# Performance work log

Measured on AMD Instinct MI355X. Metric: run time of the kernel, lower is better.

The kernel has to match this reference:

```python
import jax, jax.numpy as jnp
import numpy as np

N = 100000
F_IN = 128
DIM = 2
E = 3200000


def setup_inputs() -> dict:
    key = jax.random.key(0)
    k1, k2, k3, k4, k5, k6, k7 = jax.random.split(key, 7)
    x = jax.random.normal(k1, (N, F_IN), dtype=jnp.float32)
    edge_index = jax.random.randint(k2, (2, E), 0, N, dtype=jnp.int64)
    edge_attr = jax.random.uniform(k3, (E,), dtype=jnp.float32)
    # GCNConv params: lin weight [F_IN, DIM] (glorot), bias zeros
    conv_w = jax.random.normal(k4, (F_IN, DIM), dtype=jnp.float32) * (1.0 / np.sqrt(F_IN))
    conv_b = jnp.zeros((DIM,), dtype=jnp.float32)
    # TopKPooling score weight [DIM]
    pool_w = jax.random.normal(k5, (DIM,), dtype=jnp.float32)
    # fc: Linear(N*DIM, 1), init normal(0, 0.01), bias 0 (per init_weights)
    fc_w = jax.random.normal(k6, (N * DIM, 1), dtype=jnp.float32) * 0.01
    fc_b = jnp.zeros((1,), dtype=jnp.float32)
    return {"x": x, "edge_index": edge_index, "edge_attr": edge_attr,
            "conv_w": conv_w, "conv_b": conv_b, "pool_w": pool_w,
            "fc_w": fc_w, "fc_b": fc_b}


def reference(x, edge_index, edge_attr, conv_w, conv_b, pool_w, fc_w, fc_b):
    n = x.shape[0]
    row, col = edge_index[0], edge_index[1]
    # --- GCNConv: add self-loops (weight 1), symmetric normalization ---
    loop = jnp.arange(n, dtype=edge_index.dtype)
    row_f = jnp.concatenate([row, loop])
    col_f = jnp.concatenate([col, loop])
    w_f = jnp.concatenate([edge_attr, jnp.ones((n,), dtype=x.dtype)])
    deg = jax.ops.segment_sum(w_f, col_f, num_segments=n)  # [N]
    dinv = jnp.where(deg > 0, jax.lax.rsqrt(deg), 0.0)
    norm = dinv[row_f] * w_f * dinv[col_f]  # [E+N]
    h = x @ conv_w  # [N, DIM] transform-then-propagate
    msg = norm[:, None] * h[row_f]  # [E+N, DIM]
    out = jax.ops.segment_sum(msg, col_f, num_segments=n) + conv_b  # [N, DIM]
    # --- ReLU ---
    out = jax.nn.relu(out)
    # --- TopKPooling with k = N (single graph): score, sort desc, gate ---
    score = jnp.tanh((out @ pool_w) / jnp.linalg.norm(pool_w))  # [N]
    perm = jnp.argsort(-score)
    pooled = out[perm] * score[perm][:, None]  # [N, DIM]
    # --- flatten + fc + sigmoid ---
    flat = pooled.reshape(-1)  # [N*DIM]
    y = jax.nn.sigmoid(flat @ fc_w + fc_b)  # [1]
    return y
```

## Files before the change

### kernel.cpp

```cpp
#include <hip/hip_runtime.h>
#include <math.h>

#define FIN 128
#define W 512
#define MAXG 256
#define HB 256
#define HT 1024
#define BP 100

__device__ __forceinline__ long long edge_at(const void* p, long long i, unsigned mode) {
  return mode ? ((const long long*)p)[i] : (long long)((const int*)p)[i];
}

__device__ __forceinline__ void atomic_fadd(float* p, float v) {
  __hip_atomic_fetch_add(p, v, __ATOMIC_RELAXED, __HIP_MEMORY_SCOPE_AGENT);
}

__global__ void k_detect(const unsigned* ei, unsigned* mode, float* acc) {
  if (threadIdx.x == 0 && blockIdx.x == 0) {
    unsigned orv = 0;
    for (int i = 1; i < 1024; i += 2) orv |= ei[i];
    *mode = (orv == 0) ? 1u : 0u;
    *acc = 0.0f;
  }
}

__global__ void k_h(const float* __restrict__ x, const float* __restrict__ cw,
                    float* __restrict__ h, int n) {
  int gt = blockIdx.x * blockDim.x + threadIdx.x;
  int node = gt >> 5;
  int sub = gt & 31;
  if (node >= n) return;
  float4 xv = ((const float4*)x)[node * 32 + sub];
  float s0 = xv.x * cw[sub * 8 + 0] + xv.y * cw[sub * 8 + 2] +
             xv.z * cw[sub * 8 + 4] + xv.w * cw[sub * 8 + 6];
  float s1 = xv.x * cw[sub * 8 + 1] + xv.y * cw[sub * 8 + 3] +
             xv.z * cw[sub * 8 + 5] + xv.w * cw[sub * 8 + 7];
  for (int off = 16; off > 0; off >>= 1) {
    s0 += __shfl_down(s0, off, 32);
    s1 += __shfl_down(s1, off, 32);
  }
  if (sub == 0) { h[node * 2] = s0; h[node * 2 + 1] = s1; }
}

__global__ void k_hist(const void* ei, long long E, int G,
                       unsigned* table, const unsigned* __restrict__ mode) {
  __shared__ unsigned hist[MAXG];
  unsigned m = *mode;
  int t = threadIdx.x;
  if (t < MAXG) hist[t] = 0;
  __syncthreads();
  long long perB = (E + HB - 1) / HB;
  long long base = (long long)blockIdx.x * perB;
  long long lim = base + perB; if (lim > E) lim = E;
  for (long long e = base + t; e < lim; e += HT) {
    int c = (int)edge_at(ei, E + e, m);
    atomicAdd(&hist[c >> 9], 1u);
  }
  __syncthreads();
  if (t < G) table[(size_t)t * HB + blockIdx.x] = hist[t];
}

__global__ void k_bsum(const unsigned* __restrict__ table, unsigned* btot) {
  int b = blockIdx.x, t = threadIdx.x;
  unsigned v = table[(size_t)b * HB + t];
  for (int off = 32; off > 0; off >>= 1) v += __shfl_down(v, off);
  __shared__ unsigned wsum[4];
  if ((t & 63) == 0) wsum[t >> 6] = v;
  __syncthreads();
  if (t == 0) btot[b] = wsum[0] + wsum[1] + wsum[2] + wsum[3];
}

__global__ void k_bscan(const unsigned* __restrict__ btot, unsigned* boff,
                        int G, int chunk, unsigned total) {
  __shared__ unsigned part[256];
  int t = threadIdx.x;
  int c0 = t * chunk, c1 = c0 + chunk; if (c1 > G) c1 = G;
  unsigned s = 0;
  for (int i = c0; i < c1; ++i) s += btot[i];
  part[t] = s;
  __syncthreads();
  unsigned pre = 0;
  for (int i = 0; i < t; ++i) pre += part[i];
  unsigned run = pre;
  for (int i = c0; i < c1; ++i) { boff[i] = run; run += btot[i]; }
  if (t == 255) boff[G] = total;
}

__global__ void k_bapply(unsigned* table, const unsigned* __restrict__ boff) {
  __shared__ unsigned s[256];
  int b = blockIdx.x, t = threadIdx.x;
  unsigned v = table[(size_t)b * HB + t];
  s[t] = v;
  __syncthreads();
  for (int off = 1; off < 256; off <<= 1) {
    unsigned tmp = (t >= off) ? s[t - off] : 0u;
    __syncthreads();
    s[t] += tmp;
    __syncthreads();
  }
  table[(size_t)b * HB + t] = s[t] - v + boff[b];
}

__global__ void k_scatter(const void* ei, const float* __restrict__ attr,
                          long long E, int G, const unsigned* __restrict__ table,
                          uint2* __restrict__ packed, const unsigned* __restrict__ mode) {
  __shared__ unsigned cur[MAXG];
  unsigned m = *mode;
  int t = threadIdx.x;
  if (t < G) cur[t] = table[(size_t)t * HB + blockIdx.x];
  __syncthreads();
  long long perB = (E + HB - 1) / HB;
  long long base = (long long)blockIdx.x * perB;
  long long lim = base + perB; if (lim > E) lim = E;
  for (long long e = base + t; e < lim; e += HT) {
    int r = (int)edge_at(ei, e, m);
    int c = (int)edge_at(ei, E + e, m);
    float a = attr[e];
    unsigned pos = atomicAdd(&cur[c >> 9], 1u);
    packed[pos] = make_uint2(((unsigned)r << 9) | ((unsigned)c & 511u), __float_as_uint(a));
  }
}

__global__ void k_gdeg(const uint2* __restrict__ packed, const unsigned* __restrict__ boff,
                       float* __restrict__ deg, int n) {
  __shared__ float sdeg[W];
  int g = blockIdx.x, t = threadIdx.x;
  sdeg[t] = 1.0f;
  __syncthreads();
  unsigned s0 = boff[g], s1 = boff[g + 1];
  for (unsigned i = s0 + t; i < s1; i += W) {
    uint2 p = packed[i];
    atomicAdd(&sdeg[p.x & (W - 1u)], __uint_as_float(p.y));
  }
  __syncthreads();
  int c = g * W + t;
  if (c < n) deg[c] = sdeg[t];
}

__global__ void k_dinv(const float* __restrict__ deg, const float* __restrict__ h,
                       float* __restrict__ dinv, float* __restrict__ g, int n) {
  int i = blockIdx.x * blockDim.x + threadIdx.x;
  if (i >= n) return;
  float di = rsqrtf(deg[i]);
  dinv[i] = di;
  g[2 * i]     = di * h[2 * i];
  g[2 * i + 1] = di * h[2 * i + 1];
}

__global__ void k_gmsg(const uint2* __restrict__ packed, const unsigned* __restrict__ boff,
                       const float* __restrict__ gv, const float* __restrict__ dinv,
                       const float* __restrict__ h, const float* __restrict__ cb,
                       const float* __restrict__ pw, float* __restrict__ out,
                       float* __restrict__ score, unsigned* __restrict__ keys,
                       unsigned* __restrict__ pay, int n) {
  __shared__ float sacc[2 * W];
  int g = blockIdx.x, t = threadIdx.x;
  sacc[t] = 0.f; sacc[t + W] = 0.f;
  __syncthreads();
  unsigned s0 = boff[g], s1 = boff[g + 1];
  const float2* g2 = (const float2*)gv;
  for (unsigned i = s0 + t; i < s1; i += W) {
    uint2 p = packed[i];
    unsigned r = p.x >> 9;
    unsigned cl = p.x & (W - 1u);
    float a = __uint_as_float(p.y);
    float2 gr = g2[r];
    atomicAdd(&sacc[2 * cl],     a * gr.x);
    atomicAdd(&sacc[2 * cl + 1], a * gr.y);
  }
  __syncthreads();
  int c = g * W + t;
  if (c < n) {
    float dc = dinv[c];
    float o0 = fmaxf(dc * sacc[2 * t]     + dc * dc * h[2 * c]     + cb[0], 0.f);
    float o1 = fmaxf(dc * sacc[2 * t + 1] + dc * dc * h[2 * c + 1] + cb[1], 0.f);
    out[2 * c] = o0; out[2 * c + 1] = o1;
    float pw0 = pw[0], pw1 = pw[1];
    float s = tanhf((o0 * pw0 + o1 * pw1) / sqrtf(pw0 * pw0 + pw1 * pw1));
    score[c] = s;
    unsigned u = __float_as_uint(s);
    unsigned asc = u ^ ((u >> 31) ? 0xFFFFFFFFu : 0x80000000u);
    keys[c] = ~asc;
    pay[c] = (unsigned)c;
  }
}

__global__ void k_radix_hist(const unsigned* __restrict__ keys, int n, int shift,
                             unsigned* table) {
  __shared__ unsigned hist[256];
  int t = threadIdx.x;
  hist[t] = 0;
  __syncthreads();
  int base = blockIdx.x * 1024;
  for (int j = 0; j < 4; ++j) {
    int g = base + j * 256 + t;
    if (g < n) {
      unsigned d = (keys[g] >> shift) & 255u;
      atomicAdd(&hist[d], 1u);
    }
  }
  __syncthreads();
  table[t * BP + blockIdx.x] = hist[t];
}

__global__ void k_radix_scan(unsigned* table, int B) {
  int t = threadIdx.x;
  unsigned* row = table + t * BP;
  uint4* r4 = (uint4*)row;
  int nv = B >> 2;
  unsigned s = 0;
#pragma unroll 8
  for (int i = 0; i < nv; ++i) { uint4 v = r4[i]; s += v.x + v.y + v.z + v.w; }
  for (int i = nv * 4; i < B; ++i) s += row[i];
  int lane = t & 63, w = t >> 6;
  unsigned inc = s;
  for (int off = 1; off < 64; off <<= 1) {
    unsigned nval = __shfl_up(inc, off);
    if (lane >= off) inc += nval;
  }
  __shared__ unsigned wtot[4];
  if (lane == 63) wtot[w] = inc;
  __syncthreads();
  unsigned wpre = 0;
  for (int i = 0; i < w; ++i) wpre += wtot[i];
  unsigned run = wpre + inc - s;
#pragma unroll 8
  for (int i = 0; i < nv; ++i) {
    uint4 v = r4[i]; uint4 o;
    o.x = run; run += v.x; o.y = run; run += v.y;
    o.z = run; run += v.z; o.w = run; run += v.w;
    r4[i] = o;
  }
  for (int i = nv * 4; i < B; ++i) { unsigned v = row[i]; row[i] = run; run += v; }
}

__global__ void k_radix_scatter(const unsigned* __restrict__ keysIn,
                                const unsigned* __restrict__ payIn, int n, int shift,
                                const unsigned* __restrict__ table,
                                unsigned* keysOut, unsigned* payOut) {
  __shared__ unsigned runCnt[256];
  __shared__ unsigned waveCnt[4 * 256];
  int t = threadIdx.x;
  int lane = t & 63, w = t >> 6;
  runCnt[t] = 0;
  int base = blockIdx.x * 1024;
  for (int j = 0; j < 4; ++j) {
    for (int q = t; q < 1024; q += 256) waveCnt[q] = 0;
    __syncthreads();
    int g = base + j * 256 + t;
    bool active = g < n;
    unsigned key = 0, pay = 0, d = 0;
    if (active) { key = keysIn[g]; pay = payIn[g]; d = (key >> shift) & 255u; }
    unsigned long long am = __ballot(active);
    unsigned long long mm = ~0ull;
#pragma unroll
    for (int b = 0; b < 8; ++b) {
      unsigned long long bb = __ballot((d >> b) & 1u);
      mm &= ((d >> b) & 1u) ? bb : ~bb;
    }
    mm &= am;
    int rankw = __popcll(mm & ((1ull << lane) - 1ull));
    if (active && rankw == 0) waveCnt[w * 256 + d] = (unsigned)__popcll(mm);
    __syncthreads();
    if (active) {
      unsigned off = runCnt[d] + (unsigned)rankw;
      for (int ww = 0; ww < w; ++ww) off += waveCnt[ww * 256 + d];
      unsigned gpos = table[d * BP + blockIdx.x] + off;
      keysOut[gpos] = key;
      payOut[gpos] = pay;
    }
    __syncthreads();
    runCnt[t] += waveCnt[t] + waveCnt[256 + t] + waveCnt[512 + t] + waveCnt[768 + t];
    __syncthreads();
  }
}

__global__ void k_final(const unsigned* __restrict__ perm, const float* __restrict__ out,
                        const float* __restrict__ score, const float* __restrict__ fcw,
                        float* acc, int n) {
  int stride = gridDim.x * blockDim.x;
  float s = 0.f;
  for (int j = blockIdx.x * blockDim.x + threadIdx.x; j < n; j += stride) {
    unsigned p = perm[j];
    float sc = score[p];
    s += sc * (out[2 * p] * fcw[2 * j] + out[2 * p + 1] * fcw[2 * j + 1]);
  }
  for (int off = 32; off > 0; off >>= 1) s += __shfl_down(s, off);
  if ((threadIdx.x & 63) == 0) atomic_fadd(acc, s);
}

__global__ void k_sigmoid(const float* acc, const float* __restrict__ fcb, float* y) {
  if (threadIdx.x == 0 && blockIdx.x == 0) {
    float z = *acc + fcb[0];
    y[0] = 1.f / (1.f + expf(-z));
  }
}

extern "C" void kernel_launch(void* const* d_in, const int* in_sizes, int n_in,
                              void* d_out, int out_size, void* d_ws, size_t ws_size,
                              hipStream_t stream) {
  const float* x     = (const float*)d_in[0];
  const void*  ei    = d_in[1];
  const float* attr  = (const float*)d_in[2];
  const float* convw = (const float*)d_in[3];
  const float* convb = (const float*)d_in[4];
  const float* poolw = (const float*)d_in[5];
  const float* fcw   = (const float*)d_in[6];
  const float* fcb   = (const float*)d_in[7];
  float* y = (float*)d_out;

  int N = in_sizes[0] / FIN;
  long long E = in_sizes[2];
  int B = (N + 1023) / 1024;
  int G = (N + W - 1) / W;

  float* ws = (float*)d_ws;
  size_t off = 0;
  uint2* packed  = (uint2*)(ws + off); off += (size_t)2 * E;
  float* h       = ws + off; off += (size_t)2 * N;
  float* deg     = ws + off; off += (size_t)N;
  float* dinv    = ws + off; off += (size_t)N;
  float* gv      = ws + off; off += (size_t)2 * N;
  float* outN    = ws + off; off += (size_t)2 * N;
  float* score   = ws + off; off += (size_t)N;
  unsigned* keysA = (unsigned*)(ws + off); off += (size_t)N;
  unsigned* payA  = (unsigned*)(ws + off); off += (size_t)N;
  unsigned* keysB = (unsigned*)(ws + off); off += (size_t)N;
  unsigned* payB  = (unsigned*)(ws + off); off += (size_t)N;
  unsigned* etab  = (unsigned*)(ws + off); off += (size_t)G * HB;
  unsigned* btot  = (unsigned*)(ws + off); off += (size_t)G;
  unsigned* boff  = (unsigned*)(ws + off); off += (size_t)G + 2;
  unsigned* stab  = (unsigned*)(ws + off); off += (size_t)256 * BP;
  float* acc      = ws + off; off += 1;
  unsigned* mode  = (unsigned*)(ws + off); off += 1;

  int nb = (N + 255) / 256;
  int chunk = (G + 255) / 256;

  k_detect<<<1, 64, 0, stream>>>((const unsigned*)ei, mode, acc);
  k_h<<<(N * 32 + 255) / 256, 256, 0, stream>>>(x, convw, h, N);

  k_hist<<<HB, HT, 0, stream>>>(ei, E, G, etab, mode);
  k_bsum<<<G, 256, 0, stream>>>(etab, btot);
  k_bscan<<<1, 256, 0, stream>>>(btot, boff, G, chunk, (unsigned)E);
  k_bapply<<<G, 256, 0, stream>>>(etab, boff);
  k_scatter<<<HB, HT, 0, stream>>>(ei, attr, E, G, etab, packed, mode);

  k_gdeg<<<G, W, 0, stream>>>(packed, boff, deg, N);
  k_dinv<<<nb, 256, 0, stream>>>(deg, h, dinv, gv, N);
  k_gmsg<<<G, W, 0, stream>>>(packed, boff, gv, dinv, h, convb, poolw,
                              outN, score, keysA, payA, N);

  unsigned* ki = keysA; unsigned* pi = payA;
  unsigned* ko = keysB; unsigned* po = payB;
  for (int p = 0; p < 4; ++p) {
    int shift = 8 * p;
    k_radix_hist<<<B, 256, 0, stream>>>(ki, N, shift, stab);
    k_radix_scan<<<1, 256, 0, stream>>>(stab, B);
    k_radix_scatter<<<B, 256, 0, stream>>>(ki, pi, N, shift, stab, ko, po);
    unsigned* tk = ki; ki = ko; ko = tk;
    unsigned* tp = pi; pi = po; po = tp;
  }

  k_final<<<98, 256, 0, stream>>>(pi, outN, score, fcw, acc, N);
  k_sigmoid<<<1, 64, 0, stream>>>(acc, fcb, y);
}
```

Before: 235.5 us.

## Split group aggregation across sub-blocks and fuse radix histograms into scatter

The degree and message aggregation per 512-node group now runs on S=8 blocks each, writing partial sums that later kernels reduce. This raises parallelism beyond the roughly 196 group blocks, which were limited by per-group edge count. The block-offset scan is folded into k_bapply, and each radix scatter pass builds the next pass's histogram with global atomics, removing separate histogram kernels and launches. k_final is also vectorised and given more blocks. The cost is extra partial-sum buffer traffic and global atomics during the scatter passes.

```diff
diff --git a/kernel.cpp b/kernel.cpp
--- a/kernel.cpp
+++ b/kernel.cpp
@@ -3,6 +3,7 @@
 
 #define FIN 128
 #define W 512
+#define S 8
 #define MAXG 256
 #define HB 256
 #define HT 1024
@@ -16,13 +17,16 @@
   __hip_atomic_fetch_add(p, v, __ATOMIC_RELAXED, __HIP_MEMORY_SCOPE_AGENT);
 }
 
-__global__ void k_detect(const unsigned* ei, unsigned* mode, float* acc) {
-  if (threadIdx.x == 0 && blockIdx.x == 0) {
+__global__ void k_detect(const unsigned* ei, unsigned* mode, float* acc,
+                         unsigned* btot, int G) {
+  int t = threadIdx.x;
+  if (t == 0) {
     unsigned orv = 0;
     for (int i = 1; i < 1024; i += 2) orv |= ei[i];
     *mode = (orv == 0) ? 1u : 0u;
     *acc = 0.0f;
   }
+  for (int i = t; i < G; i += 64) btot[i] = 0;
 }
 
 __global__ void k_h(const float* __restrict__ x, const float* __restrict__ cw,
@@ -44,7 +48,8 @@
 }
 
 __global__ void k_hist(const void* ei, long long E, int G,
-                       unsigned* table, const unsigned* __restrict__ mode) {
+                       unsigned* table, unsigned* btot,
+                       const unsigned* __restrict__ mode) {
   __shared__ unsigned hist[MAXG];
   unsigned m = *mode;
   int t = threadIdx.x;
@@ -71,26 +76,21 @@
   if (t == 0) btot[b] = wsum[0] + wsum[1] + wsum[2] + wsum[3];
 }
 
-__global__ void k_bscan(const unsigned* __restrict__ btot, unsigned* boff,
-                        int G, int chunk, unsigned total) {
-  __shared__ unsigned part[256];
-  int t = threadIdx.x;
-  int c0 = t * chunk, c1 = c0 + chunk; if (c1 > G) c1 = G;
-  unsigned s = 0;
-  for (int i = c0; i < c1; ++i) s += btot[i];
-  part[t] = s;
-  __syncthreads();
-  unsigned pre = 0;
-  for (int i = 0; i < t; ++i) pre += part[i];
-  unsigned run = pre;
-  for (int i = c0; i < c1; ++i) { boff[i] = run; run += btot[i]; }
-  if (t == 255) boff[G] = total;
-}
-
-__global__ void k_bapply(unsigned* table, const unsigned* __restrict__ boff) {
+__global__ void k_bapply(unsigned* table, const unsigned* __restrict__ btot,
+                         unsigned* boff, int G, unsigned Etot) {
+  __shared__ unsigned red[256];
   __shared__ unsigned s[256];
-  int b = blockIdx.x, t = threadIdx.x;
-  unsigned v = table[(size_t)b * HB + t];
+  int g = blockIdx.x, t = threadIdx.x;
+  unsigned p = 0;
+  for (int i = t; i < g; i += 256) p += btot[i];
+  red[t] = p;
+  __syncthreads();
+  for (int off = 128; off > 0; off >>= 1) {
+    if (t < off) red[t] += red[t + off];
+    __syncthreads();
+  }
+  unsigned pre = red[0];
+  unsigned v = table[(size_t)g * HB + t];
   s[t] = v;
   __syncthreads();
   for (int off = 1; off < 256; off <<= 1) {
@@ -99,7 +99,8 @@
     s[t] += tmp;
     __syncthreads();
   }
-  table[(size_t)b * HB + t] = s[t] - v + boff[b];
+  table[(size_t)g * HB + t] = s[t] - v + pre;
+  if (t == 0) { boff[g] = pre; if (g == 0) boff[G] = Etot; }
 }
 
 __global__ void k_scatter(const void* ei, const float* __restrict__ attr,
@@ -122,45 +123,56 @@
   }
 }
 
-__global__ void k_gdeg(const uint2* __restrict__ packed, const unsigned* __restrict__ boff,
-                       float* __restrict__ deg, int n) {
+__global__ void k_pdeg(const uint2* __restrict__ packed, const unsigned* __restrict__ boff,
+                       float* __restrict__ pdeg) {
   __shared__ float sdeg[W];
-  int g = blockIdx.x, t = threadIdx.x;
-  sdeg[t] = 1.0f;
-  __syncthreads();
-  unsigned s0 = boff[g], s1 = boff[g + 1];
-  for (unsigned i = s0 + t; i < s1; i += W) {
+  int blk = blockIdx.x, t = threadIdx.x;
+  int g = blk / S, s = blk - g * S;
+  sdeg[t] = 0.f; sdeg[t + 256] = 0.f;
+  __syncthreads();
+  unsigned e0 = boff[g], e1 = boff[g + 1];
+  unsigned len = e1 - e0;
+  unsigned per = (len + S - 1) / S;
+  unsigned lo = e0 + s * per;
+  unsigned hi = lo + per; if (hi > e1) hi = e1;
+  for (unsigned i = lo + t; i < hi; i += 256) {
     uint2 p = packed[i];
     atomicAdd(&sdeg[p.x & (W - 1u)], __uint_as_float(p.y));
   }
   __syncthreads();
-  int c = g * W + t;
-  if (c < n) deg[c] = sdeg[t];
-}
-
-__global__ void k_dinv(const float* __restrict__ deg, const float* __restrict__ h,
+  pdeg[(size_t)blk * W + t] = sdeg[t];
+  pdeg[(size_t)blk * W + t + 256] = sdeg[t + 256];
+}
+
+__global__ void k_dinv(const float* __restrict__ pdeg, const float* __restrict__ h,
                        float* __restrict__ dinv, float* __restrict__ g, int n) {
   int i = blockIdx.x * blockDim.x + threadIdx.x;
   if (i >= n) return;
-  float di = rsqrtf(deg[i]);
+  int grp = i >> 9, li = i & (W - 1);
+  float d = 1.0f;
+#pragma unroll
+  for (int s = 0; s < S; ++s) d += pdeg[((size_t)(grp * S + s)) * W + li];
+  float di = rsqrtf(d);
   dinv[i] = di;
   g[2 * i]     = di * h[2 * i];
   g[2 * i + 1] = di * h[2 * i + 1];
 }
 
-__global__ void k_gmsg(const uint2* __restrict__ packed, const unsigned* __restrict__ boff,
-                       const float* __restrict__ gv, const float* __restrict__ dinv,
-                       const float* __restrict__ h, const float* __restrict__ cb,
-                       const float* __restrict__ pw, float* __restrict__ out,
-                       float* __restrict__ score, unsigned* __restrict__ keys,
-                       unsigned* __restrict__ pay, int n) {
+__global__ void k_pmsg(const uint2* __restrict__ packed, const unsigned* __restrict__ boff,
+                       const float* __restrict__ gv, float* __restrict__ pacc) {
   __shared__ float sacc[2 * W];
-  int g = blockIdx.x, t = threadIdx.x;
-  sacc[t] = 0.f; sacc[t + W] = 0.f;
-  __syncthreads();
-  unsigned s0 = boff[g], s1 = boff[g + 1];
+  int blk = blockIdx.x, t = threadIdx.x;
+  int g = blk / S, s = blk - g * S;
+#pragma unroll
+  for (int i = 0; i < 4; ++i) sacc[t + 256 * i] = 0.f;
+  __syncthreads();
+  unsigned e0 = boff[g], e1 = boff[g + 1];
+  unsigned len = e1 - e0;
+  unsigned per = (len + S - 1) / S;
+  unsigned lo = e0 + s * per;
+  unsigned hi = lo + per; if (hi > e1) hi = e1;
   const float2* g2 = (const float2*)gv;
-  for (unsigned i = s0 + t; i < s1; i += W) {
+  for (unsigned i = lo + t; i < hi; i += 256) {
     uint2 p = packed[i];
     unsigned r = p.x >> 9;
     unsigned cl = p.x & (W - 1u);
@@ -170,11 +182,28 @@
     atomicAdd(&sacc[2 * cl + 1], a * gr.y);
   }
   __syncthreads();
+#pragma unroll
+  for (int i = 0; i < 4; ++i) pacc[(size_t)blk * (2 * W) + t + 256 * i] = sacc[t + 256 * i];
+}
+
+__global__ void k_gout(const float* __restrict__ pacc, const float* __restrict__ dinv,
+                       const float* __restrict__ h, const float* __restrict__ cb,
+                       const float* __restrict__ pw, float* __restrict__ out,
+                       float* __restrict__ score, unsigned* __restrict__ keys,
+                       unsigned* __restrict__ pay, int n) {
+  int g = blockIdx.x, t = threadIdx.x;
+  const float2* p2 = (const float2*)pacc;
+  float a0 = 0.f, a1 = 0.f;
+#pragma unroll
+  for (int s = 0; s < S; ++s) {
+    float2 v = p2[(size_t)(g * S + s) * W + t];
+    a0 += v.x; a1 += v.y;
+  }
   int c = g * W + t;
   if (c < n) {
     float dc = dinv[c];
-    float o0 = fmaxf(dc * sacc[2 * t]     + dc * dc * h[2 * c]     + cb[0], 0.f);
-    float o1 = fmaxf(dc * sacc[2 * t + 1] + dc * dc * h[2 * c + 1] + cb[1], 0.f);
+    float o0 = fmaxf(dc * a0 + dc * dc * h[2 * c]     + cb[0], 0.f);
+    float o1 = fmaxf(dc * a1 + dc * dc * h[2 * c + 1] + cb[1], 0.f);
     out[2 * c] = o0; out[2 * c + 1] = o1;
     float pw0 = pw[0], pw1 = pw[1];
     float s = tanhf((o0 * pw0 + o1 * pw1) / sqrtf(pw0 * pw0 + pw1 * pw1));
@@ -186,8 +215,8 @@
   }
 }
 
-__global__ void k_radix_hist(const unsigned* __restrict__ keys, int n, int shift,
-                             unsigned* table) {
+__global__ void k_rhist0(const unsigned* __restrict__ keys, int n,
+                         unsigned* tabA, unsigned* tabB) {
   __shared__ unsigned hist[256];
   int t = threadIdx.x;
   hist[t] = 0;
@@ -195,18 +224,20 @@
   int base = blockIdx.x * 1024;
   for (int j = 0; j < 4; ++j) {
     int g = base + j * 256 + t;
-    if (g < n) {
-      unsigned d = (keys[g] >> shift) & 255u;
-      atomicAdd(&hist[d], 1u);
-    }
-  }
-  __syncthreads();
-  table[t * BP + blockIdx.x] = hist[t];
-}
-
-__global__ void k_radix_scan(unsigned* table, int B) {
-  int t = threadIdx.x;
-  unsigned* row = table + t * BP;
+    if (g < n) atomicAdd(&hist[keys[g] & 255u], 1u);
+  }
+  __syncthreads();
+  tabA[t * BP + blockIdx.x] = hist[t];
+  for (int i = blockIdx.x * 256 + t; i < 256 * BP; i += gridDim.x * 256) tabB[i] = 0;
+}
+
+__global__ void k_rscan(unsigned* tab, int B, unsigned* other) {
+  int t = threadIdx.x;
+  if (blockIdx.x == 1) {
+    if (other) for (int i = t; i < 256 * BP; i += 256) other[i] = 0;
+    return;
+  }
+  unsigned* row = tab + t * BP;
   uint4* r4 = (uint4*)row;
   int nv = B >> 2;
   unsigned s = 0;
@@ -235,10 +266,11 @@
   for (int i = nv * 4; i < B; ++i) { unsigned v = row[i]; row[i] = run; run += v; }
 }
 
-__global__ void k_radix_scatter(const unsigned* __restrict__ keysIn,
-                                const unsigned* __restrict__ payIn, int n, int shift,
-                                const unsigned* __restrict__ table,
-                                unsigned* keysOut, unsigned* payOut) {
+__global__ void k_rscatter(const unsigned* __restrict__ keysIn,
+                           const unsigned* __restrict__ payIn, int n, int shift,
+                           const unsigned* __restrict__ tabCur,
+                           unsigned* keysOut, unsigned* payOut,
+                           unsigned* tabNext) {
   __shared__ unsigned runCnt[256];
   __shared__ unsigned waveCnt[4 * 256];
   int t = threadIdx.x;
@@ -266,9 +298,13 @@
     if (active) {
       unsigned off = runCnt[d] + (unsigned)rankw;
       for (int ww = 0; ww < w; ++ww) off += waveCnt[ww * 256 + d];
-      unsigned gpos = table[d * BP + blockIdx.x] + off;
+      unsigned gpos = tabCur[d * BP + blockIdx.x] + off;
       keysOut[gpos] = key;
       payOut[gpos] = pay;
+      if (tabNext) {
+        unsigned d2 = (key >> (shift + 8)) & 255u;
+        atomicAdd(&tabNext[d2 * BP + (gpos >> 10)], 1u);
+      }
     }
     __syncthreads();
     runCnt[t] += waveCnt[t] + waveCnt[256 + t] + waveCnt[512 + t] + waveCnt[768 + t];
@@ -281,10 +317,13 @@
                         float* acc, int n) {
   int stride = gridDim.x * blockDim.x;
   float s = 0.f;
+  const float2* o2 = (const float2*)out;
+  const float2* f2 = (const float2*)fcw;
   for (int j = blockIdx.x * blockDim.x + threadIdx.x; j < n; j += stride) {
     unsigned p = perm[j];
-    float sc = score[p];
-    s += sc * (out[2 * p] * fcw[2 * j] + out[2 * p + 1] * fcw[2 * j + 1]);
+    float2 ov = o2[p];
+    float2 fv = f2[j];
+    s += score[p] * (ov.x * fv.x + ov.y * fv.y);
   }
   for (int off = 32; off > 0; off >>= 1) s += __shfl_down(s, off);
   if ((threadIdx.x & 63) == 0) atomic_fadd(acc, s);
@@ -318,8 +357,9 @@
   float* ws = (float*)d_ws;
   size_t off = 0;
   uint2* packed  = (uint2*)(ws + off); off += (size_t)2 * E;
+  float* pacc    = ws + off; off += (size_t)2 * G * S * W;
+  float* pdeg    = pacc;
   float* h       = ws + off; off += (size_t)2 * N;
-  float* deg     = ws + off; off += (size_t)N;
   float* dinv    = ws + off; off += (size_t)N;
   float* gv      = ws + off; off += (size_t)2 * N;
   float* outN    = ws + off; off += (size_t)2 * N;
@@ -331,38 +371,39 @@
   unsigned* etab  = (unsigned*)(ws + off); off += (size_t)G * HB;
   unsigned* btot  = (unsigned*)(ws + off); off += (size_t)G;
   unsigned* boff  = (unsigned*)(ws + off); off += (size_t)G + 2;
-  unsigned* stab  = (unsigned*)(ws + off); off += (size_t)256 * BP;
+  unsigned* tabA  = (unsigned*)(ws + off); off += (size_t)256 * BP;
+  unsigned* tabB  = (unsigned*)(ws + off); off += (size_t)256 * BP;
   float* acc      = ws + off; off += 1;
   unsigned* mode  = (unsigned*)(ws + off); off += 1;
 
   int nb = (N + 255) / 256;
-  int chunk = (G + 255) / 256;
-
-  k_detect<<<1, 64, 0, stream>>>((const unsigned*)ei, mode, acc);
+
+  k_detect<<<1, 64, 0, stream>>>((const unsigned*)ei, mode, acc, btot, G);
   k_h<<<(N * 32 + 255) / 256, 256, 0, stream>>>(x, convw, h, N);
 
-  k_hist<<<HB, HT, 0, stream>>>(ei, E, G, etab, mode);
+  k_hist<<<HB, HT, 0, stream>>>(ei, E, G, etab, btot, mode);
   k_bsum<<<G, 256, 0, stream>>>(etab, btot);
-  k_bscan<<<1, 256, 0, stream>>>(btot, boff, G, chunk, (unsigned)E);
-  k_bapply<<<G, 256, 0, stream>>>(etab, boff);
+  k_bapply<<<G, 256, 0, stream>>>(etab, btot, boff, G, (unsigned)E);
   k_scatter<<<HB, HT, 0, stream>>>(ei, attr, E, G, etab, packed, mode);
 
-  k_gdeg<<<G, W, 0, stream>>>(packed, boff, deg, N);
-  k_dinv<<<nb, 256, 0, stream>>>(deg, h, dinv, gv, N);
-  k_gmsg<<<G, W, 0, stream>>>(packed, boff, gv, dinv, h, convb, poolw,
-                              outN, score, keysA, payA, N);
-
+  k_pdeg<<<G * S, 256, 0, stream>>>(packed, boff, pdeg);
+  k_dinv<<<nb, 256, 0, stream>>>(pdeg, h, dinv, gv, N);
+  k_pmsg<<<G * S, 256, 0, stream>>>(packed, boff, gv, pacc);
+  k_gout<<<G, W, 0, stream>>>(pacc, dinv, h, convb, poolw, outN, score, keysA, payA, N);
+
+  k_rhist0<<<B, 256, 0, stream>>>(keysA, N, tabA, tabB);
   unsigned* ki = keysA; unsigned* pi = payA;
   unsigned* ko = keysB; unsigned* po = payB;
+  unsigned* tc = tabA;  unsigned* tn = tabB;
   for (int p = 0; p < 4; ++p) {
-    int shift = 8 * p;
-    k_radix_hist<<<B, 256, 0, stream>>>(ki, N, shift, stab);
-    k_radix_scan<<<1, 256, 0, stream>>>(stab, B);
-    k_radix_scatter<<<B, 256, 0, stream>>>(ki, pi, N, shift, stab, ko, po);
+    k_rscan<<<2, 256, 0, stream>>>(tc, B, (p == 0 || p == 3) ? (unsigned*)nullptr : tn);
+    k_rscatter<<<B, 256, 0, stream>>>(ki, pi, N, 8 * p, tc,
+                                      ko, po, (p < 3) ? tn : nullptr);
     unsigned* tk = ki; ki = ko; ko = tk;
     unsigned* tp = pi; pi = po; po = tp;
-  }
-
-  k_final<<<98, 256, 0, stream>>>(pi, outN, score, fcw, acc, N);
+    unsigned* tt = tc; tc = tn; tn = tt;
+  }
+
+  k_final<<<196, 256, 0, stream>>>(pi, outN, score, fcw, acc, N);
   k_sigmoid<<<1, 64, 0, stream>>>(acc, fcb, y);
 }
```

Result: slower. 768.4 us (+226.2%).
